# Optimization experiments

Measured on AMD Instinct MI355X. Metric: run time of the kernel, lower is better.

## Reference

```python
import jax, jax.numpy as jnp
import numpy as np

N = 2048
H = W = 128


def setup_inputs() -> dict:
    key = jax.random.key(0)
    ks = jax.random.split(key, 8)
    # Gaussians placed in front of a pinhole camera at the origin (+z forward)
    xy = jax.random.normal(ks[0], (N, 2), dtype=jnp.float32) * 1.5
    z = jax.random.uniform(ks[1], (N, 1), dtype=jnp.float32, minval=2.0, maxval=6.0)
    mean = jnp.concatenate([xy, z], axis=-1)
    qvec = jax.random.normal(ks[2], (N, 4), dtype=jnp.float32)
    # raw scales -> exp activation gives scales around 0.05
    svec_raw = jax.random.normal(ks[3], (N, 3), dtype=jnp.float32) * 0.3 - 3.0
    color_raw = jax.random.normal(ks[4], (N, 3), dtype=jnp.float32)
    alpha_raw = jax.random.normal(ks[5], (N,), dtype=jnp.float32)
    bg = jax.random.uniform(ks[6], (3,), dtype=jnp.float32)
    viewmat = jnp.eye(4, dtype=jnp.float32)
    intrins = jnp.array([120.0, 120.0, W / 2.0, H / 2.0], dtype=jnp.float32)  # fx fy cx cy
    return dict(mean=mean, qvec=qvec, svec_raw=svec_raw, color_raw=color_raw,
                alpha_raw=alpha_raw, bg=bg, viewmat=viewmat, intrins=intrins)


def _quat_to_rotmat(q):
    q = q / jnp.linalg.norm(q, axis=-1, keepdims=True)
    w, x, y, z = q[..., 0], q[..., 1], q[..., 2], q[..., 3]
    R = jnp.stack([
        1 - 2 * (y * y + z * z), 2 * (x * y - w * z), 2 * (x * z + w * y),
        2 * (x * y + w * z), 1 - 2 * (x * x + z * z), 2 * (y * z - w * x),
        2 * (x * z - w * y), 2 * (y * z + w * x), 1 - 2 * (x * x + y * y),
    ], axis=-1)
    return R.reshape(q.shape[:-1] + (3, 3))


def reference(mean, qvec, svec_raw, color_raw, alpha_raw, bg, viewmat, intrins):
    fx, fy, cx, cy = intrins[0], intrins[1], intrins[2], intrins[3]
    # activations used by GaussianSplattingRenderer (svec_act=exp, alpha/color=sigmoid)
    svec = jnp.exp(svec_raw)
    alpha = jax.nn.sigmoid(alpha_raw)
    color = jax.nn.sigmoid(color_raw)

    Rw = viewmat[:3, :3]
    tw = viewmat[:3, 3]
    p_cam = mean @ Rw.T + tw                      # (N,3)
    x, y, z = p_cam[:, 0], p_cam[:, 1], p_cam[:, 2]
    zc = jnp.maximum(z, 1e-3)

    # 3D covariance Sigma = R diag(s)^2 R^T  via  M = R diag(s),  Sigma = M M^T
    Rq = _quat_to_rotmat(qvec)                    # (N,3,3)
    M = Rq * svec[:, None, :]                     # (N,3,3)

    # perspective Jacobian (EWA splatting), composed with view rotation
    zeros = jnp.zeros_like(zc)
    J = jnp.stack([
        jnp.stack([fx / zc, zeros, -fx * x / (zc * zc)], axis=-1),
        jnp.stack([zeros, fy / zc, -fy * y / (zc * zc)], axis=-1),
    ], axis=-2)                                   # (N,2,3)
    T = jnp.einsum('nij,jk->nik', J, Rw)          # (N,2,3)
    TM = jnp.einsum('nij,njk->nik', T, M)         # (N,2,3)
    cov2d = jnp.einsum('nij,nkj->nik', TM, TM)    # (N,2,2)
    cov2d = cov2d + 0.3 * jnp.eye(2, dtype=cov2d.dtype)  # low-pass filter

    a = cov2d[:, 0, 0]; b = cov2d[:, 0, 1]; c = cov2d[:, 1, 1]
    det = a * c - b * b
    det_safe = jnp.maximum(det, 1e-8)
    conic_a = c / det_safe; conic_b = -b / det_safe; conic_c = a / det_safe

    # projected 2D means
    u = fx * x / zc + cx
    v = fy * y / zc + cy

    px = jnp.arange(W, dtype=jnp.float32) + 0.5
    py = jnp.arange(H, dtype=jnp.float32) + 0.5
    dx = px[:, None] - u[None, :]                 # (W,N)
    dy = py[:, None] - v[None, :]                 # (H,N)

    power = (-0.5 * (conic_a * dx * dx)[None, :, :]
             - 0.5 * (conic_c * dy * dy)[:, None, :]
             - conic_b[None, None, :] * dx[None, :, :] * dy[:, None, :])  # (H,W,N)
    g = jnp.exp(jnp.minimum(power, 0.0))
    valid = (z > 0.2) & (det > 0)
    alpha_pix = jnp.where(valid[None, None, :], jnp.minimum(0.99, alpha * g), 0.0)

    # front-to-back depth order, sequential alpha compositing via cumprod
    order = jnp.argsort(z)
    alpha_s = alpha_pix[:, :, order]              # (H,W,N)
    color_s = color[order]                        # (N,3)
    Tcum = jnp.cumprod(1.0 - alpha_s, axis=-1)
    Tprev = jnp.concatenate([jnp.ones_like(Tcum[..., :1]), Tcum[..., :-1]], axis=-1)
    wgt = alpha_s * Tprev                         # (H,W,N)
    img = jnp.einsum('hwn,nc->hwc', wgt, color_s) + Tcum[..., -1:] * bg
    return img
```

## Files before the change

kernel.cpp:

```cpp
#include <hip/hip_runtime.h>
#include <hip/hip_fp16.h>
#include <math.h>

#define NG 2048
#define IMG_W 128
#define IMG_H 128
#define NPIX (IMG_W * IMG_H)
#define L2E 1.4426950408889634f

struct __align__(16) PG {
    float u, v, A, B;
    float C, alpha;
    unsigned int rg;
    unsigned int b_r2;
};

__global__ __launch_bounds__(256) void prep_kernel(
    const float* __restrict__ mean, const float* __restrict__ qvec,
    const float* __restrict__ svec_raw, const float* __restrict__ color_raw,
    const float* __restrict__ alpha_raw, const float* __restrict__ viewmat,
    const float* __restrict__ intrins, PG* __restrict__ graw,
    float* __restrict__ zbuf)
{
    const int g = blockIdx.x * 256 + threadIdx.x;
    if (g >= NG) return;

    const float fx = intrins[0], fy = intrins[1], cx = intrins[2], cy = intrins[3];
    const float R00 = viewmat[0], R01 = viewmat[1], R02 = viewmat[2],  t0 = viewmat[3];
    const float R10 = viewmat[4], R11 = viewmat[5], R12 = viewmat[6],  t1 = viewmat[7];
    const float R20 = viewmat[8], R21 = viewmat[9], R22 = viewmat[10], t2 = viewmat[11];

    float mx = mean[g * 3 + 0], my = mean[g * 3 + 1], mz = mean[g * 3 + 2];
    float x = R00 * mx + R01 * my + R02 * mz + t0;
    float y = R10 * mx + R11 * my + R12 * mz + t1;
    float z = R20 * mx + R21 * my + R22 * mz + t2;
    float zc = fmaxf(z, 0.001f);

    float qw = qvec[g * 4 + 0], qx = qvec[g * 4 + 1];
    float qy = qvec[g * 4 + 2], qz = qvec[g * 4 + 3];
    float qn = rsqrtf(qw * qw + qx * qx + qy * qy + qz * qz);
    qw *= qn; qx *= qn; qy *= qn; qz *= qn;
    float Rq00 = 1.f - 2.f * (qy * qy + qz * qz), Rq01 = 2.f * (qx * qy - qw * qz), Rq02 = 2.f * (qx * qz + qw * qy);
    float Rq10 = 2.f * (qx * qy + qw * qz), Rq11 = 1.f - 2.f * (qx * qx + qz * qz), Rq12 = 2.f * (qy * qz - qw * qx);
    float Rq20 = 2.f * (qx * qz - qw * qy), Rq21 = 2.f * (qy * qz + qw * qx), Rq22 = 1.f - 2.f * (qx * qx + qy * qy);

    float s0 = expf(svec_raw[g * 3 + 0]);
    float s1 = expf(svec_raw[g * 3 + 1]);
    float s2 = expf(svec_raw[g * 3 + 2]);
    float M00 = Rq00 * s0, M01 = Rq01 * s1, M02 = Rq02 * s2;
    float M10 = Rq10 * s0, M11 = Rq11 * s1, M12 = Rq12 * s2;
    float M20 = Rq20 * s0, M21 = Rq21 * s1, M22 = Rq22 * s2;

    float iz = 1.0f / zc;
    float J00 = fx * iz, J02 = -fx * x * iz * iz;
    float J11 = fy * iz, J12 = -fy * y * iz * iz;
    float T00 = J00 * R00 + J02 * R20;
    float T01 = J00 * R01 + J02 * R21;
    float T02 = J00 * R02 + J02 * R22;
    float T10 = J11 * R10 + J12 * R20;
    float T11 = J11 * R11 + J12 * R21;
    float T12 = J11 * R12 + J12 * R22;
    float TM00 = T00 * M00 + T01 * M10 + T02 * M20;
    float TM01 = T00 * M01 + T01 * M11 + T02 * M21;
    float TM02 = T00 * M02 + T01 * M12 + T02 * M22;
    float TM10 = T10 * M00 + T11 * M10 + T12 * M20;
    float TM11 = T10 * M01 + T11 * M11 + T12 * M21;
    float TM12 = T10 * M02 + T11 * M12 + T12 * M22;
    float a = TM00 * TM00 + TM01 * TM01 + TM02 * TM02 + 0.3f;
    float b = TM00 * TM10 + TM01 * TM11 + TM02 * TM12;
    float c = TM10 * TM10 + TM11 * TM11 + TM12 * TM12 + 0.3f;
    float det = a * c - b * b;
    float det_safe = fmaxf(det, 1e-8f);
    float inv_det = 1.0f / det_safe;
    bool valid = (z > 0.2f) && (det > 0.0f);
    float alpha = 1.0f / (1.0f + expf(-alpha_raw[g]));

    float conic_a = c * inv_det;
    float conic_b = -b * inv_det;
    float conic_c = a * inv_det;

    float half_tr = 0.5f * (conic_a + conic_c);
    float half_df = 0.5f * (conic_a - conic_c);
    float lam_min = half_tr - sqrtf(half_df * half_df + conic_b * conic_b);
    float r2 = (lam_min > 1e-20f) ? (1.05f * 2.0f * 24.0f / (L2E * lam_min)) : 3.0e38f;
    if (!valid) r2 = -1.0f;

    PG pg;
    pg.u = fx * x * iz + cx;
    pg.v = fy * y * iz + cy;
    pg.A = -0.5f * L2E * conic_a;
    pg.B = -L2E * conic_b;
    pg.C = -0.5f * L2E * conic_c;
    pg.alpha = alpha;
    float cr  = 1.0f / (1.0f + expf(-color_raw[g * 3 + 0]));
    float cg  = 1.0f / (1.0f + expf(-color_raw[g * 3 + 1]));
    float cbl = 1.0f / (1.0f + expf(-color_raw[g * 3 + 2]));
    __half2 hrg = __floats2half2_rn(cr, cg);
    pg.rg = *reinterpret_cast<unsigned int*>(&hrg);
    __half2 hbr = __halves2half2(__float2half_rn(cbl), __float2half_rn(r2));
    pg.b_r2 = *reinterpret_cast<unsigned int*>(&hbr);
    graw[g] = pg;
    zbuf[g] = z;
}

__global__ __launch_bounds__(256) void rank_scatter_kernel(
    const float* __restrict__ zbuf, const PG* __restrict__ graw,
    PG* __restrict__ gsorted)
{
    const int g = (blockIdx.x * 256 + threadIdx.x) >> 6;
    const int lane = threadIdx.x & 63;
    const float zg = zbuf[g];
    const float4* z4 = (const float4*)zbuf;
    int cnt = 0;
#pragma unroll
    for (int k = 0; k < NG / 256; ++k) {
        int idx = k * 64 + lane;
        float4 zz = z4[idx];
        int h = idx * 4;
        cnt += ((zz.x < zg) || ((zz.x == zg) && (h + 0 < g))) ? 1 : 0;
        cnt += ((zz.y < zg) || ((zz.y == zg) && (h + 1 < g))) ? 1 : 0;
        cnt += ((zz.z < zg) || ((zz.z == zg) && (h + 2 < g))) ? 1 : 0;
        cnt += ((zz.w < zg) || ((zz.w == zg) && (h + 3 < g))) ? 1 : 0;
    }
#pragma unroll
    for (int off = 32; off >= 1; off >>= 1)
        cnt += __shfl_down(cnt, off);
    int rank = __shfl(cnt, 0);
    if (lane < 2) {
        ((float4*)(gsorted + rank))[lane] = ((const float4*)(graw + g))[lane];
    }
}

template <int NSEG>
__global__ __launch_bounds__(64) void composite_kernel(
    const PG* __restrict__ gsorted, float4* __restrict__ partial)
{
    constexpr int SEG = NG / NSEG;
    __shared__ float4 sg[SEG * 2];
    const int t = threadIdx.x;
    const int seg = blockIdx.z;
    const int col = blockIdx.x * 16 + (t & 15);
    const int row0 = blockIdx.y * 16 + (t >> 4) * 4;

    const float4* src = (const float4*)(gsorted + seg * SEG);
#pragma unroll
    for (int i = t; i < SEG * 2; i += 64) sg[i] = src[i];
    __syncthreads();

    const float x0 = blockIdx.x * 16 + 0.5f, x1 = x0 + 15.0f;
    const float y0 = blockIdx.y * 16 + 0.5f, y1 = y0 + 15.0f;

    const float fpx = col + 0.5f;
    const float fpy0 = row0 + 0.5f;
    float T0 = 1.f, T1 = 1.f, T2 = 1.f, T3 = 1.f;
    float Cr0 = 0.f, Cg0 = 0.f, Cb0 = 0.f;
    float Cr1 = 0.f, Cg1 = 0.f, Cb1 = 0.f;
    float Cr2 = 0.f, Cg2 = 0.f, Cb2 = 0.f;
    float Cr3 = 0.f, Cg3 = 0.f, Cb3 = 0.f;

    for (int base = 0; base < SEG; base += 64) {
        float4 g0 = sg[2 * (base + t) + 0];
        float4 g1 = sg[2 * (base + t) + 1];
        union { float f; __half2 h; } ubr; ubr.f = g1.w;
        float r2 = __half2float(__high2half(ubr.h));
        float dxm = fmaxf(0.f, fmaxf(x0 - g0.x, g0.x - x1));
        float dym = fmaxf(0.f, fmaxf(y0 - g0.y, g0.y - y1));
        bool keep = (dxm * dxm + dym * dym) <= r2;
        unsigned long long mask = __ballot(keep);

        while (mask) {
            int i = base + (int)__builtin_ctzll(mask);
            mask &= (mask - 1);
            float4 f0 = sg[2 * i + 0];
            float4 f1 = sg[2 * i + 1];
            float dx = fpx - f0.x;
            float adx2 = f0.z * dx * dx;
            float bdx = f0.w * dx;
            float alpha = f1.y;
            union { float f; __half2 h; } urg; urg.f = f1.z;
            union { float f; __half2 h; } ubl; ubl.f = f1.w;
            float cr = __half2float(__low2half(urg.h));
            float cg = __half2float(__high2half(urg.h));
            float cb = __half2float(__low2half(ubl.h));

            float dy, p, gv, a, w;

            dy = fpy0 - f0.y;
            p = fminf(fmaf(dy, fmaf(f1.x, dy, bdx), adx2), 0.f);
            gv = exp2f(p);
            a = fminf(0.99f, alpha * gv);
            w = a * T0;
            Cr0 = fmaf(w, cr, Cr0); Cg0 = fmaf(w, cg, Cg0); Cb0 = fmaf(w, cb, Cb0);
            T0 = fmaf(-a, T0, T0);

            dy = (fpy0 + 1.f) - f0.y;
            p = fminf(fmaf(dy, fmaf(f1.x, dy, bdx), adx2), 0.f);
            gv = exp2f(p);
            a = fminf(0.99f, alpha * gv);
            w = a * T1;
            Cr1 = fmaf(w, cr, Cr1); Cg1 = fmaf(w, cg, Cg1); Cb1 = fmaf(w, cb, Cb1);
            T1 = fmaf(-a, T1, T1);

            dy = (fpy0 + 2.f) - f0.y;
            p = fminf(fmaf(dy, fmaf(f1.x, dy, bdx), adx2), 0.f);
            gv = exp2f(p);
            a = fminf(0.99f, alpha * gv);
            w = a * T2;
            Cr2 = fmaf(w, cr, Cr2); Cg2 = fmaf(w, cg, Cg2); Cb2 = fmaf(w, cb, Cb2);
            T2 = fmaf(-a, T2, T2);

            dy = (fpy0 + 3.f) - f0.y;
            p = fminf(fmaf(dy, fmaf(f1.x, dy, bdx), adx2), 0.f);
            gv = exp2f(p);
            a = fminf(0.99f, alpha * gv);
            w = a * T3;
            Cr3 = fmaf(w, cr, Cr3); Cg3 = fmaf(w, cg, Cg3); Cb3 = fmaf(w, cb, Cb3);
            T3 = fmaf(-a, T3, T3);
        }
    }

    float4* dst = partial + (size_t)seg * NPIX + row0 * IMG_W + col;
    dst[0 * IMG_W] = make_float4(Cr0, Cg0, Cb0, T0);
    dst[1 * IMG_W] = make_float4(Cr1, Cg1, Cb1, T1);
    dst[2 * IMG_W] = make_float4(Cr2, Cg2, Cb2, T2);
    dst[3 * IMG_W] = make_float4(Cr3, Cg3, Cb3, T3);
}

template <int NSEG>
__global__ __launch_bounds__(64) void combine_kernel(
    const float4* __restrict__ partial, const float* __restrict__ bg,
    float* __restrict__ out)
{
    int pix = blockIdx.x * 64 + threadIdx.x;
    float T = 1.0f, Cr = 0.0f, Cg = 0.0f, Cb = 0.0f;
#pragma unroll
    for (int s = 0; s < NSEG; ++s) {
        float4 p = partial[s * NPIX + pix];
        Cr = fmaf(T, p.x, Cr);
        Cg = fmaf(T, p.y, Cg);
        Cb = fmaf(T, p.z, Cb);
        T *= p.w;
    }
    out[pix * 3 + 0] = Cr + T * bg[0];
    out[pix * 3 + 1] = Cg + T * bg[1];
    out[pix * 3 + 2] = Cb + T * bg[2];
}

template <int NSEG>
static void launch_pipeline(const float* mean, const float* qvec,
                            const float* svec_raw, const float* color_raw,
                            const float* alpha_raw, const float* bg,
                            const float* viewmat, const float* intrins,
                            float* out, char* ws, hipStream_t stream)
{
    PG* graw      = (PG*)ws;
    float* zbuf   = (float*)(ws + NG * sizeof(PG));
    PG* gsorted   = (PG*)(ws + NG * sizeof(PG) + NG * sizeof(float));
    float4* partial = (float4*)(ws + 2 * NG * sizeof(PG) + NG * sizeof(float));

    hipLaunchKernelGGL(prep_kernel, dim3(NG / 256), dim3(256), 0, stream,
                       mean, qvec, svec_raw, color_raw, alpha_raw, viewmat,
                       intrins, graw, zbuf);
    hipLaunchKernelGGL(rank_scatter_kernel, dim3(NG * 64 / 256), dim3(256),
                       0, stream, zbuf, graw, gsorted);
    hipLaunchKernelGGL((composite_kernel<NSEG>), dim3(8, 8, NSEG), dim3(64),
                       0, stream, gsorted, partial);
    hipLaunchKernelGGL((combine_kernel<NSEG>), dim3(NPIX / 64), dim3(64),
                       0, stream, partial, bg, out);
}

extern "C" void kernel_launch(void* const* d_in, const int* in_sizes, int n_in,
                              void* d_out, int out_size, void* d_ws, size_t ws_size,
                              hipStream_t stream)
{
    const float* mean      = (const float*)d_in[0];
    const float* qvec      = (const float*)d_in[1];
    const float* svec_raw  = (const float*)d_in[2];
    const float* color_raw = (const float*)d_in[3];
    const float* alpha_raw = (const float*)d_in[4];
    const float* bg        = (const float*)d_in[5];
    const float* viewmat   = (const float*)d_in[6];
    const float* intrins   = (const float*)d_in[7];
    char* ws = (char*)d_ws;
    float* out = (float*)d_out;

    const size_t fixed = 2 * NG * sizeof(PG) + NG * sizeof(float);
    if (ws_size >= fixed + (size_t)32 * NPIX * sizeof(float4)) {
        launch_pipeline<32>(mean, qvec, svec_raw, color_raw, alpha_raw, bg,
                            viewmat, intrins, out, ws, stream);
    } else if (ws_size >= fixed + (size_t)16 * NPIX * sizeof(float4)) {
        launch_pipeline<16>(mean, qvec, svec_raw, color_raw, alpha_raw, bg,
                            viewmat, intrins, out, ws, stream);
    } else {
        launch_pipeline<8>(mean, qvec, svec_raw, color_raw, alpha_raw, bg,
                           viewmat, intrins, out, ws, stream);
    }
}
```

Before: 82.83 us.

## Fuse prep with depth ranking and fold combine into composite via last-block reduction

Merges the per-Gaussian preprocessing and the depth-rank scatter into one kernel. Each wavefront now recomputes every Gaussian's camera-space depth from the means instead of reading a z buffer, and the full preprocessing is done redundantly on all 64 lanes. The separate combine kernel is replaced by an atomic per-tile counter, so the last segment block to finish for a tile merges the partials and writes the output. This cuts four launches to two, at the cost of redundant per-lane prep math, strided reads of the means, and a serialized tail reduction inside the composite grid.

```diff
diff --git a/kernel.cpp b/kernel.cpp
--- a/kernel.cpp
+++ b/kernel.cpp
@@ -15,15 +15,24 @@
     unsigned int b_r2;
 };
 
-__global__ __launch_bounds__(256) void prep_kernel(
+__device__ __forceinline__ float cam_z(float mx, float my, float mz,
+                                       float R20, float R21, float R22,
+                                       float t2)
+{
+    return fmaf(R20, mx, fmaf(R21, my, fmaf(R22, mz, t2)));
+}
+
+__global__ __launch_bounds__(256) void prep_rank_kernel(
     const float* __restrict__ mean, const float* __restrict__ qvec,
     const float* __restrict__ svec_raw, const float* __restrict__ color_raw,
     const float* __restrict__ alpha_raw, const float* __restrict__ viewmat,
-    const float* __restrict__ intrins, PG* __restrict__ graw,
-    float* __restrict__ zbuf)
-{
-    const int g = blockIdx.x * 256 + threadIdx.x;
-    if (g >= NG) return;
+    const float* __restrict__ intrins, PG* __restrict__ gsorted,
+    unsigned int* __restrict__ tile_cnt)
+{
+    const int g = (blockIdx.x * 256 + threadIdx.x) >> 6;
+    const int lane = threadIdx.x & 63;
+
+    if (blockIdx.x == 0 && threadIdx.x < 64) tile_cnt[threadIdx.x] = 0;
 
     const float fx = intrins[0], fy = intrins[1], cx = intrins[2], cy = intrins[3];
     const float R00 = viewmat[0], R01 = viewmat[1], R02 = viewmat[2],  t0 = viewmat[3];
@@ -33,7 +42,7 @@
     float mx = mean[g * 3 + 0], my = mean[g * 3 + 1], mz = mean[g * 3 + 2];
     float x = R00 * mx + R01 * my + R02 * mz + t0;
     float y = R10 * mx + R11 * my + R12 * mz + t1;
-    float z = R20 * mx + R21 * my + R22 * mz + t2;
+    float z = cam_z(mx, my, mz, R20, R21, R22, t2);
     float zc = fmaxf(z, 0.001f);
 
     float qw = qvec[g * 4 + 0], qx = qvec[g * 4 + 1];
@@ -99,41 +108,32 @@
     pg.rg = *reinterpret_cast<unsigned int*>(&hrg);
     __half2 hbr = __halves2half2(__float2half_rn(cbl), __float2half_rn(r2));
     pg.b_r2 = *reinterpret_cast<unsigned int*>(&hbr);
-    graw[g] = pg;
-    zbuf[g] = z;
-}
-
-__global__ __launch_bounds__(256) void rank_scatter_kernel(
-    const float* __restrict__ zbuf, const PG* __restrict__ graw,
-    PG* __restrict__ gsorted)
-{
-    const int g = (blockIdx.x * 256 + threadIdx.x) >> 6;
-    const int lane = threadIdx.x & 63;
-    const float zg = zbuf[g];
-    const float4* z4 = (const float4*)zbuf;
+
+    const float zg = z;
     int cnt = 0;
 #pragma unroll
-    for (int k = 0; k < NG / 256; ++k) {
-        int idx = k * 64 + lane;
-        float4 zz = z4[idx];
-        int h = idx * 4;
-        cnt += ((zz.x < zg) || ((zz.x == zg) && (h + 0 < g))) ? 1 : 0;
-        cnt += ((zz.y < zg) || ((zz.y == zg) && (h + 1 < g))) ? 1 : 0;
-        cnt += ((zz.z < zg) || ((zz.z == zg) && (h + 2 < g))) ? 1 : 0;
-        cnt += ((zz.w < zg) || ((zz.w == zg) && (h + 3 < g))) ? 1 : 0;
+    for (int k = 0; k < NG / 64; ++k) {
+        int h = k * 64 + lane;
+        float hx = mean[h * 3 + 0], hy = mean[h * 3 + 1], hz = mean[h * 3 + 2];
+        float zh = cam_z(hx, hy, hz, R20, R21, R22, t2);
+        cnt += ((zh < zg) || ((zh == zg) && (h < g))) ? 1 : 0;
     }
 #pragma unroll
     for (int off = 32; off >= 1; off >>= 1)
         cnt += __shfl_down(cnt, off);
     int rank = __shfl(cnt, 0);
+
     if (lane < 2) {
-        ((float4*)(gsorted + rank))[lane] = ((const float4*)(graw + g))[lane];
+        const float4* src = reinterpret_cast<const float4*>(&pg);
+        ((float4*)(gsorted + rank))[lane] = src[lane];
     }
 }
 
 template <int NSEG>
 __global__ __launch_bounds__(64) void composite_kernel(
-    const PG* __restrict__ gsorted, float4* __restrict__ partial)
+    const PG* __restrict__ gsorted, float4* __restrict__ partial,
+    unsigned int* __restrict__ tile_cnt, const float* __restrict__ bg,
+    float* __restrict__ out)
 {
     constexpr int SEG = NG / NSEG;
     __shared__ float4 sg[SEG * 2];
@@ -224,26 +224,33 @@
     dst[1 * IMG_W] = make_float4(Cr1, Cg1, Cb1, T1);
     dst[2 * IMG_W] = make_float4(Cr2, Cg2, Cb2, T2);
     dst[3 * IMG_W] = make_float4(Cr3, Cg3, Cb3, T3);
-}
-
-template <int NSEG>
-__global__ __launch_bounds__(64) void combine_kernel(
-    const float4* __restrict__ partial, const float* __restrict__ bg,
-    float* __restrict__ out)
-{
-    int pix = blockIdx.x * 64 + threadIdx.x;
-    float T = 1.0f, Cr = 0.0f, Cg = 0.0f, Cb = 0.0f;
-#pragma unroll
-    for (int s = 0; s < NSEG; ++s) {
-        float4 p = partial[s * NPIX + pix];
-        Cr = fmaf(T, p.x, Cr);
-        Cg = fmaf(T, p.y, Cg);
-        Cb = fmaf(T, p.z, Cb);
-        T *= p.w;
-    }
-    out[pix * 3 + 0] = Cr + T * bg[0];
-    out[pix * 3 + 1] = Cg + T * bg[1];
-    out[pix * 3 + 2] = Cb + T * bg[2];
+
+    __threadfence();
+    int old;
+    const int tile = blockIdx.y * 8 + blockIdx.x;
+    if (t == 0) old = (int)atomicAdd(&tile_cnt[tile], 1u);
+    old = __shfl(old, 0);
+    if (old == NSEG - 1) {
+        __threadfence();
+        const float bg0 = bg[0], bg1 = bg[1], bg2 = bg[2];
+        const int pixbase = row0 * IMG_W + col;
+#pragma unroll
+        for (int r = 0; r < 4; ++r) {
+            const int pix = pixbase + r * IMG_W;
+            float T = 1.f, Cr = 0.f, Cg = 0.f, Cb = 0.f;
+#pragma unroll
+            for (int s = 0; s < NSEG; ++s) {
+                float4 p = partial[(size_t)s * NPIX + pix];
+                Cr = fmaf(T, p.x, Cr);
+                Cg = fmaf(T, p.y, Cg);
+                Cb = fmaf(T, p.z, Cb);
+                T *= p.w;
+            }
+            out[pix * 3 + 0] = Cr + T * bg0;
+            out[pix * 3 + 1] = Cg + T * bg1;
+            out[pix * 3 + 2] = Cb + T * bg2;
+        }
+    }
 }
 
 template <int NSEG>
@@ -253,20 +260,16 @@
                             const float* viewmat, const float* intrins,
                             float* out, char* ws, hipStream_t stream)
 {
-    PG* graw      = (PG*)ws;
-    float* zbuf   = (float*)(ws + NG * sizeof(PG));
-    PG* gsorted   = (PG*)(ws + NG * sizeof(PG) + NG * sizeof(float));
-    float4* partial = (float4*)(ws + 2 * NG * sizeof(PG) + NG * sizeof(float));
-
-    hipLaunchKernelGGL(prep_kernel, dim3(NG / 256), dim3(256), 0, stream,
-                       mean, qvec, svec_raw, color_raw, alpha_raw, viewmat,
-                       intrins, graw, zbuf);
-    hipLaunchKernelGGL(rank_scatter_kernel, dim3(NG * 64 / 256), dim3(256),
-                       0, stream, zbuf, graw, gsorted);
+    PG* gsorted = (PG*)ws;
+    float4* partial = (float4*)(ws + NG * sizeof(PG));
+    unsigned int* tile_cnt =
+        (unsigned int*)(ws + NG * sizeof(PG) + (size_t)NSEG * NPIX * sizeof(float4));
+
+    hipLaunchKernelGGL(prep_rank_kernel, dim3(NG * 64 / 256), dim3(256), 0,
+                       stream, mean, qvec, svec_raw, color_raw, alpha_raw,
+                       viewmat, intrins, gsorted, tile_cnt);
     hipLaunchKernelGGL((composite_kernel<NSEG>), dim3(8, 8, NSEG), dim3(64),
-                       0, stream, gsorted, partial);
-    hipLaunchKernelGGL((combine_kernel<NSEG>), dim3(NPIX / 64), dim3(64),
-                       0, stream, partial, bg, out);
+                       0, stream, gsorted, partial, tile_cnt, bg, out);
 }
 
 extern "C" void kernel_launch(void* const* d_in, const int* in_sizes, int n_in,
@@ -284,7 +287,7 @@
     char* ws = (char*)d_ws;
     float* out = (float*)d_out;
 
-    const size_t fixed = 2 * NG * sizeof(PG) + NG * sizeof(float);
+    const size_t fixed = NG * sizeof(PG) + 64 * sizeof(unsigned int);
     if (ws_size >= fixed + (size_t)32 * NPIX * sizeof(float4)) {
         launch_pipeline<32>(mean, qvec, svec_raw, color_raw, alpha_raw, bg,
                             viewmat, intrins, out, ws, stream);
```

Result: slower. 161.1 us (+94.5%).
